# Performance work log

Hardware: AMD Instinct MI355X
Metric: run time of the kernel (lower is better)

Reference implementation:

```python
import jax, jax.numpy as jnp
import numpy as np

B, T, E = 2, 2048, 1024
H, D = 16, 64          # num_heads, head_dim (v_head_dim == head_dim)


def setup_inputs() -> dict:
    key = jax.random.key(0)
    ks = jax.random.split(key, 10)
    s = lambda fan_in: 1.0 / np.sqrt(fan_in)
    inp = {
        "embed": jax.random.normal(ks[0], (B, T, E), dtype=jnp.float32),
        "mask": jax.random.randint(ks[1], (B, T, T), 0, 2) > 0,
        # Linear weights stored as [in, out] (y = x @ W + b)
        "Wq": jax.random.uniform(ks[2], (E, H * D), minval=-s(E), maxval=s(E)),
        "bq": jnp.zeros((H * D,), jnp.float32),
        "Wk": jax.random.uniform(ks[3], (E, H * D), minval=-s(E), maxval=s(E)),
        "bk": jnp.zeros((H * D,), jnp.float32),
        "Wv": jax.random.uniform(ks[4], (E, H * D), minval=-s(E), maxval=s(E)),
        "bv": jnp.zeros((H * D,), jnp.float32),
        "Wz": jax.random.uniform(ks[5], (H * D, E), minval=-s(H * D), maxval=s(H * D)),
        "bz": jnp.zeros((E,), jnp.float32),
    }
    return inp


def reference(embed, mask, Wq, bq, Wk, bk, Wv, bv, Wz, bz):
    # Self-attention: context = embed
    q = (embed @ Wq + bq).reshape(B, T, H, D)   # b t h d
    k = (embed @ Wk + bk).reshape(B, T, H, D)   # b T h d
    v = (embed @ Wv + bv).reshape(B, T, H, D)   # b T h d

    scale = D ** (-0.5)
    score = jnp.einsum('bthd,bThd->bhtT', q, k) * scale   # [b,h,t,T] materialized, as in source
    max_neg = -jnp.finfo(score.dtype).max
    score = jnp.where(mask[:, None, :, :], score, max_neg)
    norm_score = jax.nn.softmax(score, axis=-1)
    z = jnp.einsum('bhtT,bThd->bthd', norm_score, v)      # [b,t,h,d]
    flat_z = z.reshape(B, T, H * D)
    return flat_z @ Wz + bz
```

## Files before the change

kernel.cpp:

```cpp
#include <hip/hip_runtime.h>
#include <hip/hip_bf16.h>


typedef __bf16 bf8_t  __attribute__((ext_vector_type(8)));
typedef __bf16 bf4_t  __attribute__((ext_vector_type(4)));
typedef float  f4_t   __attribute__((ext_vector_type(4)));

constexpr int Bb = 2, Tt = 2048, Hh = 16, Dd = 64;

#define ASYNC16(g, l)                                                        \
    __builtin_amdgcn_global_load_lds(                                        \
        (const __attribute__((address_space(1))) void*)(g),                  \
        (__attribute__((address_space(3))) void*)(l), 16, 0, 0)

#if __has_builtin(__builtin_amdgcn_exp2f)
#define EXP2F(x) __builtin_amdgcn_exp2f(x)
#else
#define EXP2F(x) exp2f(x)
#endif

__global__ __launch_bounds__(256) void convert_kernel(
    const float* __restrict__ in, __bf16* __restrict__ out)
{
    int i = (blockIdx.x * 256 + threadIdx.x) * 4;
    float4 v = *reinterpret_cast<const float4*>(in + i);
    bf4_t o = {(__bf16)v.x, (__bf16)v.y, (__bf16)v.z, (__bf16)v.w};
    *reinterpret_cast<bf4_t*>(out + i) = o;
}

__global__ __launch_bounds__(256) void maskbias_kernel(
    const int* __restrict__ m, __bf16* __restrict__ o)
{
    int i = (blockIdx.x * 256 + threadIdx.x) * 4;
    int4 v = *reinterpret_cast<const int4*>(m + i);
    const __bf16 z = (__bf16)0.f, neg = (__bf16)(-1e30f);
    bf4_t r = {v.x ? z : neg, v.y ? z : neg, v.z ? z : neg, v.w ? z : neg};
    *reinterpret_cast<bf4_t*>(o + i) = r;
}

__global__ __launch_bounds__(256) void transpose_kernel(
    const float* __restrict__ w0, const float* __restrict__ w1,
    const float* __restrict__ w2, const float* __restrict__ w3,
    __bf16* __restrict__ o0, __bf16* __restrict__ o1,
    __bf16* __restrict__ o2, __bf16* __restrict__ o3)
{
    const float* in; __bf16* out;
    switch (blockIdx.z) {
        case 0: in = w0; out = o0; break;
        case 1: in = w1; out = o1; break;
        case 2: in = w2; out = o2; break;
        default: in = w3; out = o3; break;
    }
    __shared__ float t[32][33];
    int x  = threadIdx.x & 31;
    int y0 = threadIdx.x >> 5;
    int bx = blockIdx.x * 32;
    int by = blockIdx.y * 32;
    #pragma unroll
    for (int i = 0; i < 4; i++) {
        int y = y0 + i * 8;
        t[y][x] = in[(size_t)(by + y) * 1024 + bx + x];
    }
    __syncthreads();
    #pragma unroll
    for (int i = 0; i < 4; i++) {
        int y = y0 + i * 8;
        out[(size_t)(bx + y) * 1024 + by + x] = (__bf16)t[x][y];
    }
}

template <int TM, typename OutT>
__device__ __forceinline__ void gemm_body(const __bf16* __restrict__ A,
                                          const __bf16* __restrict__ Bt,
                                          const float* __restrict__ bias,
                                          OutT* __restrict__ out,
                                          int mode, float oscale, int bx, int by)
{
    constexpr int NI = TM / 32;
    alignas(16) __shared__ __bf16 As[TM * 64];
    alignas(16) __shared__ __bf16 Bs[128 * 64];

    int tid  = threadIdx.x;
    int lane = tid & 63;
    int quad = lane >> 4;
    int l16  = lane & 15;
    int wave = tid >> 6;
    int wm   = wave >> 1, wn = wave & 1;

    f4_t acc[NI][4];
    #pragma unroll
    for (int i = 0; i < NI; i++)
        #pragma unroll
        for (int j = 0; j < 4; j++)
            acc[i][j] = f4_t{0.f, 0.f, 0.f, 0.f};

    for (int kt = 0; kt < 1024; kt += 64) {
        #pragma unroll
        for (int i = 0; i < TM / 32; i++) {
            int c   = tid + 256 * i;
            int row = c >> 3, j = c & 7;
            ASYNC16(A + (size_t)(by * TM + row) * 1024 + kt + ((j ^ (row & 7)) * 8),
                    &As[c * 8]);
        }
        #pragma unroll
        for (int i = 0; i < 4; i++) {
            int c   = tid + 256 * i;
            int row = c >> 3, j = c & 7;
            ASYNC16(Bt + (size_t)(bx * 128 + row) * 1024 + kt + ((j ^ (row & 7)) * 8),
                    &Bs[c * 8]);
        }
        __syncthreads();

        bf8_t af[2][NI], bfr[2][4];
        #pragma unroll
        for (int c = 0; c < 2; c++) {
            #pragma unroll
            for (int im = 0; im < NI; im++) {
                int row = wm * (TM / 2) + im * 16 + l16;
                af[c][im] = *reinterpret_cast<const bf8_t*>(
                    &As[row * 64 + (((c * 4 + quad) ^ (row & 7)) * 8)]);
            }
            #pragma unroll
            for (int in_ = 0; in_ < 4; in_++) {
                int row = wn * 64 + in_ * 16 + l16;
                bfr[c][in_] = *reinterpret_cast<const bf8_t*>(
                    &Bs[row * 64 + (((c * 4 + quad) ^ (row & 7)) * 8)]);
            }
        }
        #pragma unroll
        for (int c = 0; c < 2; c++)
            #pragma unroll
            for (int im = 0; im < NI; im++)
                #pragma unroll
                for (int in_ = 0; in_ < 4; in_++)
                    acc[im][in_] = __builtin_amdgcn_mfma_f32_16x16x32_bf16(
                        af[c][im], bfr[c][in_], acc[im][in_], 0, 0, 0);
        __syncthreads();
    }

    #pragma unroll
    for (int im = 0; im < NI; im++) {
        #pragma unroll
        for (int in_ = 0; in_ < 4; in_++) {
            int gc  = bx * 128 + wn * 64 + in_ * 16 + l16;
            float bb = bias[gc];
            int gr0 = by * TM + wm * (TM / 2) + im * 16 + quad * 4;
            #pragma unroll
            for (int r = 0; r < 4; r++) {
                int gr  = gr0 + r;
                float v = (acc[im][in_][r] + bb) * oscale;
                size_t idx;
                if (mode == 0) {
                    idx = (size_t)gr * 1024 + gc;
                } else {
                    int b = gr >> 11, t = gr & 2047;
                    int h = gc >> 6,  d = gc & 63;
                    if (mode == 1) idx = ((size_t)(b * Hh + h) * Tt + t) * Dd + d;
                    else           idx = ((size_t)(b * Hh + h) * Dd + d) * Tt + t;
                }
                out[idx] = (OutT)v;
            }
        }
    }
}

__global__ __launch_bounds__(256) void gemm_qkv_kernel(
    const __bf16* __restrict__ A,
    const __bf16* __restrict__ WqT, const __bf16* __restrict__ WkT, const __bf16* __restrict__ WvT,
    const float* __restrict__ bq,  const float* __restrict__ bk,  const float* __restrict__ bv,
    __bf16* __restrict__ Qo, __bf16* __restrict__ Ko, __bf16* __restrict__ Vo)
{
    const __bf16* Bt; const float* bias; __bf16* out; int mode; float sc;
    if      (blockIdx.z == 0) { Bt = WqT; bias = bq; out = Qo; mode = 1; sc = 0.18033688011112042f; }
    else if (blockIdx.z == 1) { Bt = WkT; bias = bk; out = Ko; mode = 1; sc = 1.f; }
    else                      { Bt = WvT; bias = bv; out = Vo; mode = 2; sc = 1.f; }
    gemm_body<128, __bf16>(A, Bt, bias, out, mode, sc, blockIdx.x, blockIdx.y);
}

__global__ __launch_bounds__(256) void gemm_out_kernel(
    const __bf16* __restrict__ A, const __bf16* __restrict__ Bt,
    const float* __restrict__ bias, float* __restrict__ out)
{
    gemm_body<64, float>(A, Bt, bias, out, 0, 1.f, blockIdx.x, blockIdx.y);
}

__global__ __launch_bounds__(512, 4) void flash_kernel(
    const __bf16* __restrict__ Qb, const __bf16* __restrict__ Kb,
    const __bf16* __restrict__ Vb, const __bf16* __restrict__ biasb,
    __bf16* __restrict__ Zb)
{
    alignas(16) __shared__ __bf16 Ks[2][64 * 64];
    alignas(16) __shared__ __bf16 Vs[2][64 * 64];
    alignas(16) __shared__ __bf16 Ps[8 * 16 * 72];

    int tid  = threadIdx.x;
    int lane = tid & 63;
    int wave = tid >> 6;
    int quad = lane >> 4;
    int l16  = lane & 15;
    int b = blockIdx.z, h = blockIdx.y;
    int bh = b * Hh + h;
    int qrow = blockIdx.x * 128 + wave * 16;

    int srow = tid >> 3, sj = tid & 7;
    const __bf16* kgp = Kb + ((size_t)bh * Tt + srow) * Dd + ((sj ^ (srow & 7)) * 8);
    const __bf16* vgp = Vb + ((size_t)bh * Dd + srow) * Tt + ((sj ^ (srow & 7)) * 8);
    const int sdst = tid * 8;

    bf8_t qf[2];
    #pragma unroll
    for (int c = 0; c < 2; c++)
        qf[c] = *reinterpret_cast<const bf8_t*>(
            Qb + ((size_t)bh * Tt + qrow + l16) * Dd + c * 32 + quad * 8);

    const __bf16* bp = biasb + ((size_t)b * Tt + qrow + l16) * Tt + quad * 4;

    float l_i = 0.f;
    f4_t o[4];
    #pragma unroll
    for (int d = 0; d < 4; d++) o[d] = f4_t{0.f, 0.f, 0.f, 0.f};

    __bf16* pw = Ps + wave * 16 * 72;

    bf8_t kreg = *reinterpret_cast<const bf8_t*>(kgp);
    bf8_t vreg = *reinterpret_cast<const bf8_t*>(vgp);
    bf4_t breg[4];
    #pragma unroll
    for (int n = 0; n < 4; n++)
        breg[n] = *reinterpret_cast<const bf4_t*>(bp + n * 16);

    for (int kt = 0; kt < Tt; kt += 64) {
        int par = (kt >> 6) & 1;
        *reinterpret_cast<bf8_t*>(&Ks[par][sdst]) = kreg;
        *reinterpret_cast<bf8_t*>(&Vs[par][sdst]) = vreg;
        f4_t s[4];
        #pragma unroll
        for (int n = 0; n < 4; n++)
            s[n] = f4_t{(float)breg[n][0], (float)breg[n][1],
                        (float)breg[n][2], (float)breg[n][3]};
        __syncthreads();

        int ktn = (kt + 64 < Tt) ? kt + 64 : 0;
        kreg = *reinterpret_cast<const bf8_t*>(kgp + (size_t)ktn * Dd);
        vreg = *reinterpret_cast<const bf8_t*>(vgp + ktn);
        #pragma unroll
        for (int n = 0; n < 4; n++)
            breg[n] = *reinterpret_cast<const bf4_t*>(bp + ktn + n * 16);

        #pragma unroll
        for (int c = 0; c < 2; c++)
            #pragma unroll
            for (int n = 0; n < 4; n++) {
                int krow = n * 16 + l16;
                bf8_t kf = *reinterpret_cast<const bf8_t*>(
                    &Ks[par][krow * 64 + (((c * 4 + quad) ^ (krow & 7)) * 8)]);
                s[n] = __builtin_amdgcn_mfma_f32_16x16x32_bf16(kf, qf[c], s[n], 0, 0, 0);
            }

        float rs = 0.f;
        #pragma unroll
        for (int n = 0; n < 4; n++) {
            bf4_t pv4;
            #pragma unroll
            for (int r = 0; r < 4; r++) {
                float p = EXP2F(s[n][r]);
                rs += p;
                pv4[r] = (__bf16)p;
            }
            *reinterpret_cast<bf4_t*>(&pw[l16 * 72 + n * 16 + quad * 4]) = pv4;
        }
        rs += __shfl_xor(rs, 16);
        rs += __shfl_xor(rs, 32);
        l_i += rs;

        #pragma unroll
        for (int c = 0; c < 2; c++) {
            bf8_t pf = *reinterpret_cast<const bf8_t*>(
                &pw[l16 * 72 + c * 32 + quad * 8]);
            #pragma unroll
            for (int ds = 0; ds < 4; ds++) {
                int vrow = ds * 16 + l16;
                bf8_t vf = *reinterpret_cast<const bf8_t*>(
                    &Vs[par][vrow * 64 + (((c * 4 + quad) ^ (vrow & 7)) * 8)]);
                o[ds] = __builtin_amdgcn_mfma_f32_16x16x32_bf16(vf, pf, o[ds], 0, 0, 0);
            }
        }
    }

    float inv = 1.f / fmaxf(l_i, 1e-30f);
    size_t zrow = ((size_t)b * Tt + qrow + l16) * 1024 + h * 64;
    #pragma unroll
    for (int ds = 0; ds < 4; ds++) {
        bf4_t ov;
        #pragma unroll
        for (int r = 0; r < 4; r++) ov[r] = (__bf16)(o[ds][r] * inv);
        *reinterpret_cast<bf4_t*>(Zb + zrow + ds * 16 + quad * 4) = ov;
    }
}

extern "C" void kernel_launch(void* const* d_in, const int* in_sizes, int n_in,
                              void* d_out, int out_size, void* d_ws, size_t ws_size,
                              hipStream_t stream)
{
    (void)in_sizes; (void)n_in; (void)out_size; (void)ws_size;

    const float* embed = (const float*)d_in[0];
    const int*   mask  = (const int*)d_in[1];
    const float* Wq = (const float*)d_in[2];
    const float* bq = (const float*)d_in[3];
    const float* Wk = (const float*)d_in[4];
    const float* bk = (const float*)d_in[5];
    const float* Wv = (const float*)d_in[6];
    const float* bv = (const float*)d_in[7];
    const float* Wz = (const float*)d_in[8];
    const float* bz = (const float*)d_in[9];
    float* out = (float*)d_out;

    char* ws = (char*)d_ws;
    const size_t MB = (size_t)1024 * 1024;
    __bf16* WqT = (__bf16*)(ws + 0 * MB);
    __bf16* WkT = (__bf16*)(ws + 2 * MB);
    __bf16* WvT = (__bf16*)(ws + 4 * MB);
    __bf16* WzT = (__bf16*)(ws + 6 * MB);
    __bf16* Eb  = (__bf16*)(ws + 8 * MB);
    __bf16* Qb  = (__bf16*)(ws + 16 * MB);
    __bf16* Kb  = (__bf16*)(ws + 24 * MB);
    __bf16* Vb  = (__bf16*)(ws + 32 * MB);
    __bf16* Zb  = (__bf16*)(ws + 40 * MB);
    __bf16* Mb  = (__bf16*)(ws + 48 * MB);

    convert_kernel<<<dim3(4096), 256, 0, stream>>>(embed, Eb);
    maskbias_kernel<<<dim3(8192), 256, 0, stream>>>(mask, Mb);
    transpose_kernel<<<dim3(32, 32, 4), 256, 0, stream>>>(Wq, Wk, Wv, Wz,
                                                          WqT, WkT, WvT, WzT);
    gemm_qkv_kernel<<<dim3(8, 32, 3), 256, 0, stream>>>(Eb, WqT, WkT, WvT,
                                                        bq, bk, bv, Qb, Kb, Vb);
    flash_kernel<<<dim3(16, Hh, Bb), 512, 0, stream>>>(Qb, Kb, Vb, Mb, Zb);
    gemm_out_kernel<<<dim3(8, 64, 1), 256, 0, stream>>>(Zb, WzT, bz, out);
}
```

Measured before the change: 244.0 us.

## Split flash attention over key dimension and combine partial results in a new kernel

The flash kernel now splits the key range into two halves, doubling the grid from 512 to 1024 blocks. Each block writes unnormalized fp32 partial outputs and row sums, and a new combine kernel adds them and normalizes into the bf16 Z buffer. The LDS double-buffer is dropped for a single buffer with an extra barrier per tile, and launch bounds are raised to 8 blocks per CU. This targets low occupancy and too few blocks on the CU count, at the cost of an extra launch, about 32MB of fp32 partial traffic, and loss of the LDS double buffering.

Result: slower. 282.6 us (+15.8%).

```diff
diff --git a/kernel.cpp b/kernel.cpp
--- a/kernel.cpp
+++ b/kernel.cpp
@@ -184,13 +184,13 @@
     gemm_body<64, float>(A, Bt, bias, out, 0, 1.f, blockIdx.x, blockIdx.y);
 }
 
-__global__ __launch_bounds__(512, 4) void flash_kernel(
+__global__ __launch_bounds__(512, 8) void flash_kernel(
     const __bf16* __restrict__ Qb, const __bf16* __restrict__ Kb,
     const __bf16* __restrict__ Vb, const __bf16* __restrict__ biasb,
-    __bf16* __restrict__ Zb)
-{
-    alignas(16) __shared__ __bf16 Ks[2][64 * 64];
-    alignas(16) __shared__ __bf16 Vs[2][64 * 64];
+    float* __restrict__ Opart, float* __restrict__ Lpart)
+{
+    alignas(16) __shared__ __bf16 Ks[64 * 64];
+    alignas(16) __shared__ __bf16 Vs[64 * 64];
     alignas(16) __shared__ __bf16 Ps[8 * 16 * 72];
 
     int tid  = threadIdx.x;
@@ -198,13 +198,16 @@
     int wave = tid >> 6;
     int quad = lane >> 4;
     int l16  = lane & 15;
-    int b = blockIdx.z, h = blockIdx.y;
-    int bh = b * Hh + h;
+    int b    = blockIdx.z >> 1;
+    int split= blockIdx.z & 1;
+    int h    = blockIdx.y;
+    int bh   = b * Hh + h;
     int qrow = blockIdx.x * 128 + wave * 16;
+    const int kt0 = split * 1024;
 
     int srow = tid >> 3, sj = tid & 7;
-    const __bf16* kgp = Kb + ((size_t)bh * Tt + srow) * Dd + ((sj ^ (srow & 7)) * 8);
-    const __bf16* vgp = Vb + ((size_t)bh * Dd + srow) * Tt + ((sj ^ (srow & 7)) * 8);
+    const __bf16* kgp = Kb + ((size_t)bh * Tt + kt0 + srow) * Dd + ((sj ^ (srow & 7)) * 8);
+    const __bf16* vgp = Vb + ((size_t)bh * Dd + srow) * Tt + kt0 + ((sj ^ (srow & 7)) * 8);
     const int sdst = tid * 8;
 
     bf8_t qf[2];
@@ -213,7 +216,7 @@
         qf[c] = *reinterpret_cast<const bf8_t*>(
             Qb + ((size_t)bh * Tt + qrow + l16) * Dd + c * 32 + quad * 8);
 
-    const __bf16* bp = biasb + ((size_t)b * Tt + qrow + l16) * Tt + quad * 4;
+    const __bf16* bp = biasb + ((size_t)b * Tt + qrow + l16) * Tt + kt0 + quad * 4;
 
     float l_i = 0.f;
     f4_t o[4];
@@ -229,10 +232,9 @@
     for (int n = 0; n < 4; n++)
         breg[n] = *reinterpret_cast<const bf4_t*>(bp + n * 16);
 
-    for (int kt = 0; kt < Tt; kt += 64) {
-        int par = (kt >> 6) & 1;
-        *reinterpret_cast<bf8_t*>(&Ks[par][sdst]) = kreg;
-        *reinterpret_cast<bf8_t*>(&Vs[par][sdst]) = vreg;
+    for (int kt = 0; kt < 1024; kt += 64) {
+        *reinterpret_cast<bf8_t*>(&Ks[sdst]) = kreg;
+        *reinterpret_cast<bf8_t*>(&Vs[sdst]) = vreg;
         f4_t s[4];
         #pragma unroll
         for (int n = 0; n < 4; n++)
@@ -240,7 +242,7 @@
                         (float)breg[n][2], (float)breg[n][3]};
         __syncthreads();
 
-        int ktn = (kt + 64 < Tt) ? kt + 64 : 0;
+        int ktn = (kt + 64 < 1024) ? kt + 64 : 0;
         kreg = *reinterpret_cast<const bf8_t*>(kgp + (size_t)ktn * Dd);
         vreg = *reinterpret_cast<const bf8_t*>(vgp + ktn);
         #pragma unroll
@@ -253,7 +255,7 @@
             for (int n = 0; n < 4; n++) {
                 int krow = n * 16 + l16;
                 bf8_t kf = *reinterpret_cast<const bf8_t*>(
-                    &Ks[par][krow * 64 + (((c * 4 + quad) ^ (krow & 7)) * 8)]);
+                    &Ks[krow * 64 + (((c * 4 + quad) ^ (krow & 7)) * 8)]);
                 s[n] = __builtin_amdgcn_mfma_f32_16x16x32_bf16(kf, qf[c], s[n], 0, 0, 0);
             }
 
@@ -281,21 +283,37 @@
             for (int ds = 0; ds < 4; ds++) {
                 int vrow = ds * 16 + l16;
                 bf8_t vf = *reinterpret_cast<const bf8_t*>(
-                    &Vs[par][vrow * 64 + (((c * 4 + quad) ^ (vrow & 7)) * 8)]);
+                    &Vs[vrow * 64 + (((c * 4 + quad) ^ (vrow & 7)) * 8)]);
                 o[ds] = __builtin_amdgcn_mfma_f32_16x16x32_bf16(vf, pf, o[ds], 0, 0, 0);
             }
         }
-    }
-
-    float inv = 1.f / fmaxf(l_i, 1e-30f);
-    size_t zrow = ((size_t)b * Tt + qrow + l16) * 1024 + h * 64;
-    #pragma unroll
-    for (int ds = 0; ds < 4; ds++) {
-        bf4_t ov;
-        #pragma unroll
-        for (int r = 0; r < 4; r++) ov[r] = (__bf16)(o[ds][r] * inv);
-        *reinterpret_cast<bf4_t*>(Zb + zrow + ds * 16 + quad * 4) = ov;
-    }
+        __syncthreads();
+    }
+
+    size_t orow = ((size_t)(split * Bb + b) * Tt + qrow + l16) * 1024 + h * 64;
+    #pragma unroll
+    for (int ds = 0; ds < 4; ds++)
+        *reinterpret_cast<f4_t*>(Opart + orow + ds * 16 + quad * 4) = o[ds];
+    if (quad == 0)
+        Lpart[((size_t)(split * Bb + b) * Tt + qrow + l16) * Hh + h] = l_i;
+}
+
+__global__ __launch_bounds__(256) void combine_kernel(
+    const float* __restrict__ Opart, const float* __restrict__ Lpart,
+    __bf16* __restrict__ Zb)
+{
+    const size_t NTOT = (size_t)Bb * Tt * 1024;
+    size_t i = ((size_t)blockIdx.x * 256 + threadIdx.x) * 4;
+    size_t row = i >> 10;
+    int    h   = (int)((i & 1023) >> 6);
+    f4_t a = *reinterpret_cast<const f4_t*>(Opart + i);
+    f4_t c = *reinterpret_cast<const f4_t*>(Opart + NTOT + i);
+    float l = Lpart[row * Hh + h] + Lpart[(size_t)Bb * Tt * Hh + row * Hh + h];
+    float inv = 1.f / fmaxf(l, 1e-30f);
+    bf4_t ov;
+    #pragma unroll
+    for (int r = 0; r < 4; r++) ov[r] = (__bf16)((a[r] + c[r]) * inv);
+    *reinterpret_cast<bf4_t*>(Zb + i) = ov;
 }
 
 extern "C" void kernel_launch(void* const* d_in, const int* in_sizes, int n_in,
@@ -328,6 +346,8 @@
     __bf16* Vb  = (__bf16*)(ws + 32 * MB);
     __bf16* Zb  = (__bf16*)(ws + 40 * MB);
     __bf16* Mb  = (__bf16*)(ws + 48 * MB);
+    float*  Op  = (float*)(ws + 64 * MB);
+    float*  Lp  = (float*)(ws + 96 * MB);
 
     convert_kernel<<<dim3(4096), 256, 0, stream>>>(embed, Eb);
     maskbias_kernel<<<dim3(8192), 256, 0, stream>>>(mask, Mb);
@@ -335,6 +355,7 @@
                                                           WqT, WkT, WvT, WzT);
     gemm_qkv_kernel<<<dim3(8, 32, 3), 256, 0, stream>>>(Eb, WqT, WkT, WvT,
                                                         bq, bk, bv, Qb, Kb, Vb);
-    flash_kernel<<<dim3(16, Hh, Bb), 512, 0, stream>>>(Qb, Kb, Vb, Mb, Zb);
+    flash_kernel<<<dim3(16, Hh, Bb * 2), 512, 0, stream>>>(Qb, Kb, Vb, Mb, Op, Lp);
+    combine_kernel<<<dim3(4096), 256, 0, stream>>>(Op, Lp, Zb);
     gemm_out_kernel<<<dim3(8, 64, 1), 256, 0, stream>>>(Zb, WzT, bz, out);
 }
```

## Fuse mask conversion into flash kernel and vectorize transposed V store

Applied to the files above, without the earlier changes.

Drops the separate mask-to-bf16-bias pre-pass. The flash attention kernel now reads the int32 mask directly and builds the -1e30/0 bias in registers, which removes one full read and write pass over the mask plus a kernel launch. In exchange, each flash block loads 16-byte int4 mask chunks instead of 8-byte bf16 ones, doubling the mask bytes it pulls through cache across all heads. Separately, the QKV GEMM epilogue for the transposed V layout now packs four consecutive t values into one bf4 store instead of four scalar stores.

Result: faster. 238.2 us (-2.4%).

```diff
diff --git a/kernel.cpp b/kernel.cpp
--- a/kernel.cpp
+++ b/kernel.cpp
@@ -26,16 +26,6 @@
     float4 v = *reinterpret_cast<const float4*>(in + i);
     bf4_t o = {(__bf16)v.x, (__bf16)v.y, (__bf16)v.z, (__bf16)v.w};
     *reinterpret_cast<bf4_t*>(out + i) = o;
-}
-
-__global__ __launch_bounds__(256) void maskbias_kernel(
-    const int* __restrict__ m, __bf16* __restrict__ o)
-{
-    int i = (blockIdx.x * 256 + threadIdx.x) * 4;
-    int4 v = *reinterpret_cast<const int4*>(m + i);
-    const __bf16 z = (__bf16)0.f, neg = (__bf16)(-1e30f);
-    bf4_t r = {v.x ? z : neg, v.y ? z : neg, v.z ? z : neg, v.w ? z : neg};
-    *reinterpret_cast<bf4_t*>(o + i) = r;
 }
 
 __global__ __launch_bounds__(256) void transpose_kernel(
@@ -145,20 +135,30 @@
             int gc  = bx * 128 + wn * 64 + in_ * 16 + l16;
             float bb = bias[gc];
             int gr0 = by * TM + wm * (TM / 2) + im * 16 + quad * 4;
-            #pragma unroll
-            for (int r = 0; r < 4; r++) {
-                int gr  = gr0 + r;
-                float v = (acc[im][in_][r] + bb) * oscale;
-                size_t idx;
-                if (mode == 0) {
-                    idx = (size_t)gr * 1024 + gc;
-                } else {
-                    int b = gr >> 11, t = gr & 2047;
-                    int h = gc >> 6,  d = gc & 63;
-                    if (mode == 1) idx = ((size_t)(b * Hh + h) * Tt + t) * Dd + d;
-                    else           idx = ((size_t)(b * Hh + h) * Dd + d) * Tt + t;
+            if (mode == 2) {
+                int b = gr0 >> 11, t0 = gr0 & 2047;
+                int h = gc >> 6,  d = gc & 63;
+                bf4_t ov;
+                #pragma unroll
+                for (int r = 0; r < 4; r++)
+                    ov[r] = (__bf16)(acc[im][in_][r] + bb);
+                *reinterpret_cast<bf4_t*>(
+                    (__bf16*)out + ((size_t)(b * Hh + h) * Dd + d) * Tt + t0) = ov;
+            } else {
+                #pragma unroll
+                for (int r = 0; r < 4; r++) {
+                    int gr  = gr0 + r;
+                    float v = (acc[im][in_][r] + bb) * oscale;
+                    size_t idx;
+                    if (mode == 0) {
+                        idx = (size_t)gr * 1024 + gc;
+                    } else {
+                        int b = gr >> 11, t = gr & 2047;
+                        int h = gc >> 6,  d = gc & 63;
+                        idx = ((size_t)(b * Hh + h) * Tt + t) * Dd + d;
+                    }
+                    out[idx] = (OutT)v;
                 }
-                out[idx] = (OutT)v;
             }
         }
     }
@@ -186,7 +186,7 @@
 
 __global__ __launch_bounds__(512, 4) void flash_kernel(
     const __bf16* __restrict__ Qb, const __bf16* __restrict__ Kb,
-    const __bf16* __restrict__ Vb, const __bf16* __restrict__ biasb,
+    const __bf16* __restrict__ Vb, const int* __restrict__ mask,
     __bf16* __restrict__ Zb)
 {
     alignas(16) __shared__ __bf16 Ks[2][64 * 64];
@@ -213,7 +213,7 @@
         qf[c] = *reinterpret_cast<const bf8_t*>(
             Qb + ((size_t)bh * Tt + qrow + l16) * Dd + c * 32 + quad * 8);
 
-    const __bf16* bp = biasb + ((size_t)b * Tt + qrow + l16) * Tt + quad * 4;
+    const int* mp = mask + ((size_t)b * Tt + qrow + l16) * Tt + quad * 4;
 
     float l_i = 0.f;
     f4_t o[4];
@@ -224,10 +224,10 @@
 
     bf8_t kreg = *reinterpret_cast<const bf8_t*>(kgp);
     bf8_t vreg = *reinterpret_cast<const bf8_t*>(vgp);
-    bf4_t breg[4];
+    int4 ireg[4];
     #pragma unroll
     for (int n = 0; n < 4; n++)
-        breg[n] = *reinterpret_cast<const bf4_t*>(bp + n * 16);
+        ireg[n] = *reinterpret_cast<const int4*>(mp + n * 16);
 
     for (int kt = 0; kt < Tt; kt += 64) {
         int par = (kt >> 6) & 1;
@@ -236,8 +236,8 @@
         f4_t s[4];
         #pragma unroll
         for (int n = 0; n < 4; n++)
-            s[n] = f4_t{(float)breg[n][0], (float)breg[n][1],
-                        (float)breg[n][2], (float)breg[n][3]};
+            s[n] = f4_t{ireg[n].x ? 0.f : -1e30f, ireg[n].y ? 0.f : -1e30f,
+                        ireg[n].z ? 0.f : -1e30f, ireg[n].w ? 0.f : -1e30f};
         __syncthreads();
 
         int ktn = (kt + 64 < Tt) ? kt + 64 : 0;
@@ -245,7 +245,7 @@
         vreg = *reinterpret_cast<const bf8_t*>(vgp + ktn);
         #pragma unroll
         for (int n = 0; n < 4; n++)
-            breg[n] = *reinterpret_cast<const bf4_t*>(bp + ktn + n * 16);
+            ireg[n] = *reinterpret_cast<const int4*>(mp + ktn + n * 16);
 
         #pragma unroll
         for (int c = 0; c < 2; c++)
@@ -327,14 +327,12 @@
     __bf16* Kb  = (__bf16*)(ws + 24 * MB);
     __bf16* Vb  = (__bf16*)(ws + 32 * MB);
     __bf16* Zb  = (__bf16*)(ws + 40 * MB);
-    __bf16* Mb  = (__bf16*)(ws + 48 * MB);
 
     convert_kernel<<<dim3(4096), 256, 0, stream>>>(embed, Eb);
-    maskbias_kernel<<<dim3(8192), 256, 0, stream>>>(mask, Mb);
     transpose_kernel<<<dim3(32, 32, 4), 256, 0, stream>>>(Wq, Wk, Wv, Wz,
                                                           WqT, WkT, WvT, WzT);
     gemm_qkv_kernel<<<dim3(8, 32, 3), 256, 0, stream>>>(Eb, WqT, WkT, WvT,
                                                         bq, bk, bv, Qb, Kb, Vb);
-    flash_kernel<<<dim3(16, Hh, Bb), 512, 0, stream>>>(Qb, Kb, Vb, Mb, Zb);
+    flash_kernel<<<dim3(16, Hh, Bb), 512, 0, stream>>>(Qb, Kb, Vb, mask, Zb);
     gemm_out_kernel<<<dim3(8, 64, 1), 256, 0, stream>>>(Zb, WzT, bz, out);
 }
```
